# Performance work log

Measured on AMD Instinct MI355X. Metric: run time of the kernel, lower is better.

Reference implementation:

```python
import jax, jax.numpy as jnp
import numpy as np


def setup_inputs() -> dict:
    key = jax.random.key(0)
    ks = jax.random.split(key, 6)
    B, N, F = 32, 1000, 256
    x = jax.random.normal(ks[0], (B, N, F), jnp.float32)
    num_nodes = jax.random.randint(ks[1], (B,), 500, N + 1, dtype=jnp.int32)
    num_sentences = jax.random.randint(ks[2], (B,), 10, 100, dtype=jnp.int32)
    valid = (jnp.arange(N)[None, :] < num_nodes[:, None]).astype(jnp.float32)
    # sparse-like weighted adjacency (avg degree ~20), zeroed on padded rows/cols
    w = jax.random.uniform(ks[3], (B, N, N), jnp.float32)
    m = (jax.random.uniform(ks[4], (B, N, N)) < 0.02).astype(jnp.float32)
    adj = w * m * valid[:, :, None] * valid[:, None, :]
    W = jax.random.normal(ks[5], (F, 1), jnp.float32) * 0.1
    b = jnp.zeros((1,), jnp.float32)
    return dict(x=x, adj=adj, W=W, b=b, num_nodes=num_nodes,
                num_sentences=num_sentences, num_output_sentences=3)


def reference(x, adj, W, b, num_nodes, num_sentences, num_output_sentences):
    B, N, F = x.shape
    I = jnp.eye(N, dtype=x.dtype)
    valid = jnp.arange(N)[None, :] < num_nodes[:, None]  # [B,N]

    # --- GCNConv attention: sym-normalized (A_bin + I), out dim 1 ---
    A_bin = (adj > 0).astype(x.dtype)
    A_hat = A_bin + I
    dis = A_hat.sum(-1) ** -0.5  # deg >= 1 from self loops
    norm = dis[:, :, None] * A_hat * dis[:, None, :]
    alpha = jnp.einsum('bnm,bmf,fo->bno', norm, x, W)[..., 0] + b[0]
    alpha = jax.nn.sigmoid(alpha ** 2)           # pow(.,2) then sigmoid
    alpha = jnp.where(valid, alpha, -1.0)        # padded nodes sort last, cut to 0

    # --- top-k cutoff: keep highest-alpha nodes until num_output_sentences
    # sentence nodes (node index < num_sentences) have been seen ---
    order = jnp.argsort(-alpha, axis=-1)                      # descending
    is_sent = (order < num_sentences[:, None]).astype(jnp.int32)
    cum = jnp.cumsum(is_sent, axis=-1)
    cut_pos = jnp.argmax(cum >= num_output_sentences, axis=-1)  # first hit
    cut_node = jnp.take_along_axis(order, cut_pos[:, None], axis=1)
    cut_value = jnp.take_along_axis(alpha, cut_node, axis=1)     # [B,1]
    cut_alpha = jax.nn.relu(alpha + 1e-7 - cut_value)
    rank_mask = (jnp.arange(N)[None, :] <= cut_pos[:, None]).astype(x.dtype)
    index_mask = jnp.zeros_like(alpha).at[jnp.arange(B)[:, None], order].set(rank_mask)

    # --- normalize_batch_adj on the weighted adjacency ---
    A2 = adj + I
    d2 = jnp.clip(A2.sum(-1), 1.0) ** -0.5
    normA = d2[:, :, None] * A2 * d2[:, None, :]
    normA = (adj.sum(-1) > 0).astype(x.dtype)[:, :, None] * normA

    # --- assignment matrix S = row-L1-normalized (normA * cut_alpha[cols]) ---
    S = normA * cut_alpha[:, None, :]
    S = S / jnp.clip(jnp.sum(jnp.abs(S), axis=-1, keepdims=True), 1e-12)

    # --- coarsen: x' = S^T x ; A' = floor(S^T A S * 1e4)/1e4 ---
    x_c = jnp.einsum('bni,bnf->bif', S, x)
    coarse_adj = jnp.einsum('bim,bmj->bij', jnp.einsum('bni,bnm->bim', S, adj), S)
    coarse_adj = jnp.floor(coarse_adj * 1e4) / 1e4
    return x_c, coarse_adj, S, index_mask
```

## Files before the change

### kernel.cpp

```cpp
#include <hip/hip_runtime.h>
#include <math.h>
#include <limits.h>

#define CAP 64
#define TPB 256
#define RPB 4
#define NMAX 1024

typedef float f4 __attribute__((ext_vector_type(4)));

__device__ inline f4 ntload4(const float* p) { return __builtin_nontemporal_load((const f4*)p); }
__device__ inline void ntstore4(float* p, f4 v) { __builtin_nontemporal_store(v, (f4*)p); }
__device__ inline void ntstore1(float* p, float v) { __builtin_nontemporal_store(v, p); }

__device__ inline float waveSum(float v) {
#pragma unroll
  for (int o = 32; o > 0; o >>= 1) v += __shfl_down(v, o, 64);
  return v;
}

__global__ void k_prep(const float* __restrict__ x, const float* __restrict__ adj,
                       const float* __restrict__ W, float* __restrict__ y,
                       int* __restrict__ rowCnt, int* __restrict__ rowIdx,
                       float* __restrict__ rowVal, float* __restrict__ dis,
                       float* __restrict__ d2, float* __restrict__ wsum,
                       int* __restrict__ colCount, int* __restrict__ colK,
                       int N, int F, int BN, int B) {
  int wave = threadIdx.x >> 6, lane = threadIdx.x & 63;
  if (blockIdx.x == 0 && threadIdx.x < B) colK[threadIdx.x] = 0;
  int bn = blockIdx.x * RPB + wave;
  if (bn >= BN) return;
  if (lane == 0) colCount[bn] = 0;
  float p = 0.f;
  if ((F & 3) == 0) {
    const float* xr = x + (size_t)bn * F;
    int f4n = F >> 2;
    for (int i = lane; i < f4n; i += 64) {
      f4 a = *(const f4*)(xr + 4 * i);
      f4 w = *(const f4*)(W + 4 * i);
      p += a.x * w.x + a.y * w.y + a.z * w.z + a.w * w.w;
    }
  } else {
    for (int f = lane; f < F; f += 64) p += x[(size_t)bn * F + f] * W[f];
  }
  float ydot = waveSum(p);
  const float* row = adj + (size_t)bn * N;
  size_t lbase = (size_t)bn * CAP;
  unsigned long long below = (1ULL << lane) - 1ULL;
  float ls = 0.f;
  int cnt = 0;
  if ((N & 3) == 0) {
    int n4 = N >> 2;
    for (int q = lane; q < n4; q += 64) {
      f4 v = ntload4(row + 4 * q);
      ls += v.x + v.y + v.z + v.w;
      int j = q << 2;
#pragma unroll
      for (int c = 0; c < 4; c++) {
        float vc = (c == 0) ? v.x : (c == 1) ? v.y : (c == 2) ? v.z : v.w;
        unsigned long long m = __ballot(vc > 0.f);
        if (vc > 0.f) {
          int pos = cnt + __popcll(m & below);
          if (pos < CAP) { rowIdx[lbase + pos] = j + c; rowVal[lbase + pos] = vc; }
        }
        cnt += __popcll(m);
      }
    }
  } else {
    for (int j = lane; j < N; j += 64) {
      float v = row[j];
      ls += v;
      unsigned long long m = __ballot(v > 0.f);
      if (v > 0.f) {
        int pos = cnt + __popcll(m & below);
        if (pos < CAP) { rowIdx[lbase + pos] = j; rowVal[lbase + pos] = v; }
      }
      cnt += __popcll(m);
    }
  }
  float s = waveSum(ls);
  if (lane == 0) {
    y[bn] = ydot;
    rowCnt[bn] = cnt;
    dis[bn] = 1.f / sqrtf((float)(cnt + 1));
    wsum[bn] = s;
    d2[bn] = 1.f / sqrtf(fmaxf(s + 1.f, 1.f));
  }
}

__global__ void k_alpha(const float* __restrict__ adj, const int* __restrict__ rowCnt,
                        const int* __restrict__ rowIdx, const float* __restrict__ dis,
                        const float* __restrict__ y, const float* __restrict__ bptr,
                        const int* __restrict__ num_nodes, float* __restrict__ alpha,
                        int N, int BN) {
  int wave = threadIdx.x >> 6, lane = threadIdx.x & 63;
  int bn = blockIdx.x * RPB + wave;
  if (bn >= BN) return;
  int b = bn / N, n = bn - b * N;
  const float* disB = dis + (size_t)b * N;
  const float* yB = y + (size_t)b * N;
  int cnt = rowCnt[bn];
  float acc = 0.f;
  if (cnt <= CAP) {
    for (int t = lane; t < cnt; t += 64) {
      int j = rowIdx[(size_t)bn * CAP + t];
      acc += disB[j] * yB[j];
    }
  } else {
    const float* row = adj + (size_t)bn * N;
    for (int j = lane; j < N; j += 64)
      if (row[j] > 0.f) acc += disB[j] * yB[j];
  }
  float tot = waveSum(acc);
  if (lane == 0) {
    float dn = dis[bn];
    tot += dn * yB[n];
    float z = dn * tot + bptr[0];
    float a;
    if (n < num_nodes[b]) { float z2 = z * z; a = 1.f / (1.f + expf(-z2)); }
    else a = -1.f;
    alpha[bn] = a;
  }
}

__global__ void k_cut(const float* __restrict__ alpha, const int* __restrict__ num_sentences,
                      const int* __restrict__ kptr, float* __restrict__ cutA,
                      float* __restrict__ outIM, int* __restrict__ colK,
                      int* __restrict__ colIdx, int N) {
  int b = blockIdx.x;
  const float* aB = alpha + (size_t)b * N;
  __shared__ float s_cutv;
  __shared__ int s_cutn;
  if (threadIdx.x < 64) {
    int lane = threadIdx.x;
    int ns = num_sentences[b];
    int k = kptr[0];
    if (k < 1) k = 1;
    if (k > ns) k = ns;
    unsigned long long used = 0ULL;
    float cv = 0.f; int cn = 0;
    int nslots = (ns + 63) >> 6;
    for (int r = 0; r < k; r++) {
      float bv = -3.4e38f; int bi = INT_MAX;
      for (int s = 0; s < nslots; s++) {
        int idx = lane + (s << 6);
        if (idx < ns && !((used >> s) & 1ULL)) {
          float v = aB[idx];
          if (v > bv || (v == bv && idx < bi)) { bv = v; bi = idx; }
        }
      }
#pragma unroll
      for (int o = 32; o > 0; o >>= 1) {
        float ov = __shfl_down(bv, o, 64);
        int oi = __shfl_down(bi, o, 64);
        if (ov > bv || (ov == bv && oi < bi)) { bv = ov; bi = oi; }
      }
      bv = __shfl(bv, 0, 64);
      bi = __shfl(bi, 0, 64);
      if ((bi & 63) == lane) used |= 1ULL << (bi >> 6);
      cv = bv; cn = bi;
    }
    if (lane == 0) { s_cutv = cv; s_cutn = cn; }
  }
  __syncthreads();
  float cutv = s_cutv;
  int cutn = s_cutn;
  for (int n = threadIdx.x; n < N; n += TPB) {
    float a = aB[n];
    float ca = fmaxf((a + 1e-7f) - cutv, 0.f);
    cutA[(size_t)b * N + n] = ca;
    ntstore1(&outIM[(size_t)b * N + n], (a > cutv || (a == cutv && n <= cutn)) ? 1.f : 0.f);
    if (ca > 0.f) {
      int p = atomicAdd(&colK[b], 1);
      colIdx[(size_t)b * N + p] = n;
    }
  }
}

__global__ void k_srow(const float* __restrict__ adj, const int* __restrict__ rowCnt,
                       const int* __restrict__ rowIdx, const float* __restrict__ rowVal,
                       const float* __restrict__ wsum, const float* __restrict__ d2,
                       const float* __restrict__ cutA, float* __restrict__ outS,
                       int* __restrict__ colCount, int* __restrict__ colR,
                       float* __restrict__ colV, int N, int BN) {
  int wave = threadIdx.x >> 6, lane = threadIdx.x & 63;
  int bn = blockIdx.x * RPB + wave;
  bool rowOK = bn < BN;
  __shared__ float srow[RPB][NMAX];
  float* my = srow[wave];
  if (rowOK) for (int j = lane; j < N; j += 64) my[j] = 0.f;
  if (rowOK && wsum[bn] > 0.f) {
    int b = bn / N, n = bn - b * N;
    int cnt = rowCnt[bn];
    const float* d2B = d2 + (size_t)b * N;
    const float* caB = cutA + (size_t)b * N;
    float d2n = d2[bn];
    if (cnt < CAP) {
      int t = lane;
      int j = -1; float a2 = 0.f;
      if (t < cnt) {
        j = rowIdx[(size_t)bn * CAP + t];
        float v = rowVal[(size_t)bn * CAP + t];
        a2 = v + (j == n ? 1.f : 0.f);
      }
      unsigned long long hasDiag = __ballot(t < cnt && j == n);
      if (t == cnt && hasDiag == 0ULL) { j = n; a2 = 1.f; }
      float sun = 0.f;
      if (j >= 0) {
        float ca = caB[j];
        if (ca > 0.f) sun = d2n * a2 * d2B[j] * ca;
        else j = -1;
      }
      float denom = __shfl(waveSum(sun), 0, 64);
      denom = fmaxf(denom, 1e-12f);
      if (j >= 0) {
        float s = sun / denom;
        my[j] = s;
        int cp = atomicAdd(&colCount[(size_t)b * N + j], 1);
        if (cp < CAP) {
          colR[((size_t)b * N + j) * CAP + cp] = n;
          colV[((size_t)b * N + j) * CAP + cp] = s;
        }
      }
    } else {
      const float* row = adj + (size_t)bn * N;
      float ls = 0.f;
      for (int j2 = lane; j2 < N; j2 += 64) {
        float v = row[j2];
        bool nz = (v > 0.f) || (j2 == n);
        float a2 = v + (j2 == n ? 1.f : 0.f);
        float ca = caB[j2];
        if (nz && ca > 0.f) ls += d2n * a2 * d2B[j2] * ca;
      }
      float denom = __shfl(waveSum(ls), 0, 64);
      denom = fmaxf(denom, 1e-12f);
      for (int j2 = lane; j2 < N; j2 += 64) {
        float v = row[j2];
        bool nz = (v > 0.f) || (j2 == n);
        float a2 = v + (j2 == n ? 1.f : 0.f);
        float ca = caB[j2];
        if (nz && ca > 0.f) {
          float s = (d2n * a2 * d2B[j2] * ca) / denom;
          my[j2] = s;
          int cp = atomicAdd(&colCount[(size_t)b * N + j2], 1);
          if (cp < CAP) {
            colR[((size_t)b * N + j2) * CAP + cp] = n;
            colV[((size_t)b * N + j2) * CAP + cp] = s;
          }
        }
      }
    }
  }
  if (rowOK) {
    float* dst = outS + (size_t)bn * N;
    if ((N & 3) == 0) {
      int nq = N >> 2;
      for (int q = lane; q < nq; q += 64) {
        f4 v = { my[4 * q], my[4 * q + 1], my[4 * q + 2], my[4 * q + 3] };
        ntstore4(dst + 4 * q, v);
      }
    } else {
      for (int j = lane; j < N; j += 64) ntstore1(&dst[j], my[j]);
    }
  }
}

__global__ void k_coarse(const float* __restrict__ adj, const float* __restrict__ x,
                         const float* __restrict__ cutA,
                         const int* __restrict__ rowCnt, const int* __restrict__ rowIdx,
                         const float* __restrict__ rowVal,
                         const int* __restrict__ colK, const int* __restrict__ colIdx,
                         const int* __restrict__ colCount, const int* __restrict__ colR,
                         const float* __restrict__ colV,
                         float* __restrict__ outXc, float* __restrict__ outC,
                         int N, int F) {
  int bn = blockIdx.x;
  int b = bn / N;
  float* xcRow = outXc + (size_t)bn * F;
  float* cRow = outC + (size_t)bn * N;
  bool v4N = (N & 3) == 0, v4F = (F & 3) == 0;
  int nq = N >> 2, fq = F >> 2;
  if (cutA[bn] <= 0.f) {
    f4 z4 = { 0.f, 0.f, 0.f, 0.f };
    if (v4F) for (int q = threadIdx.x; q < fq; q += TPB) ntstore4(xcRow + 4 * q, z4);
    else for (int f = threadIdx.x; f < F; f += TPB) ntstore1(&xcRow[f], 0.f);
    if (v4N) for (int q = threadIdx.x; q < nq; q += TPB) ntstore4(cRow + 4 * q, z4);
    else for (int j = threadIdx.x; j < N; j += TPB) ntstore1(&cRow[j], 0.f);
    return;
  }
  __shared__ float T[NMAX];
  __shared__ float crow[NMAX];
  __shared__ int eR[CAP];
  __shared__ float eV[CAP];
  __shared__ int eCnt[CAP];
  int cci = colCount[bn];
  if (cci > CAP) cci = CAP;
  for (int r = threadIdx.x; r < cci; r += TPB) {
    int n_r = colR[(size_t)bn * CAP + r];
    eR[r] = n_r;
    eV[r] = colV[(size_t)bn * CAP + r];
    eCnt[r] = rowCnt[(size_t)b * N + n_r];
  }
  for (int m = threadIdx.x; m < N; m += TPB) { T[m] = 0.f; crow[m] = 0.f; }
  __syncthreads();
  const float* xB = x + (size_t)b * N * F;
  for (int f = threadIdx.x; f < F; f += TPB) {
    float acc = 0.f;
    for (int r = 0; r < cci; r++) acc += eV[r] * xB[(size_t)eR[r] * F + f];
    ntstore1(&xcRow[f], acc);
  }
  for (int idx = threadIdx.x; idx < cci * CAP; idx += TPB) {
    int r = idx >> 6;
    int t = idx & (CAP - 1);
    int c = eCnt[r];
    if (c <= CAP && t < c) {
      size_t base = ((size_t)b * N + eR[r]) * CAP;
      atomicAdd(&T[rowIdx[base + t]], eV[r] * rowVal[base + t]);
    }
  }
  for (int r = 0; r < cci; r++) {
    if (eCnt[r] > CAP) {
      const float* arow = adj + ((size_t)b * N + eR[r]) * N;
      float v = eV[r];
      for (int m = threadIdx.x; m < N; m += TPB) {
        float a = arow[m];
        if (a != 0.f) atomicAdd(&T[m], v * a);
      }
    }
  }
  __syncthreads();
  int K = colK[b];
  for (int jj = threadIdx.x; jj < K; jj += TPB) {
    int j = colIdx[(size_t)b * N + jj];
    int cj = colCount[(size_t)b * N + j];
    if (cj > CAP) cj = CAP;
    const int* jR = colR + ((size_t)b * N + j) * CAP;
    const float* jV = colV + ((size_t)b * N + j) * CAP;
    float cc = 0.f;
    for (int p = 0; p < cj; p++) cc += T[jR[p]] * jV[p];
    crow[j] = floorf(cc * 1e4f) / 1e4f;
  }
  __syncthreads();
  if (v4N) {
    for (int q = threadIdx.x; q < nq; q += TPB) {
      f4 v = { crow[4 * q], crow[4 * q + 1], crow[4 * q + 2], crow[4 * q + 3] };
      ntstore4(cRow + 4 * q, v);
    }
  } else {
    for (int j = threadIdx.x; j < N; j += TPB) ntstore1(&cRow[j], crow[j]);
  }
}

extern "C" void kernel_launch(void* const* d_in, const int* in_sizes, int n_in,
                              void* d_out, int out_size, void* d_ws, size_t ws_size,
                              hipStream_t stream) {
  const float* x = (const float*)d_in[0];
  const float* adj = (const float*)d_in[1];
  const float* W = (const float*)d_in[2];
  const float* bias = (const float*)d_in[3];
  const int* num_nodes = (const int*)d_in[4];
  const int* num_sentences = (const int*)d_in[5];
  const int* kptr = (const int*)d_in[6];

  int F = in_sizes[2];
  int B = in_sizes[4];
  int N = (int)(in_sizes[0] / ((long long)B * F));
  size_t BN = (size_t)B * N;

  float* outXc = (float*)d_out;
  float* outC = outXc + BN * F;
  float* outS = outC + BN * N;
  float* outIM = outS + BN * N;

  char* p = (char*)d_ws;
  auto alloc = [&](size_t bytes) -> void* {
    void* r = (void*)p;
    p += (bytes + 255) / 256 * 256;
    return r;
  };
  float* y = (float*)alloc(BN * 4);
  float* dis = (float*)alloc(BN * 4);
  float* d2 = (float*)alloc(BN * 4);
  float* wsum = (float*)alloc(BN * 4);
  float* alpha = (float*)alloc(BN * 4);
  float* cutA = (float*)alloc(BN * 4);
  int* rowCnt = (int*)alloc(BN * 4);
  int* rowIdx = (int*)alloc(BN * CAP * 4);
  float* rowVal = (float*)alloc(BN * CAP * 4);
  int* colCount = (int*)alloc(BN * 4);
  int* colR = (int*)alloc(BN * CAP * 4);
  float* colV = (float*)alloc(BN * CAP * 4);
  int* colK = (int*)alloc(B * 4);
  int* colIdx = (int*)alloc(BN * 4);

  int BNi = (int)BN;
  int rowBlocks = (BNi + RPB - 1) / RPB;
  k_prep<<<dim3(rowBlocks), dim3(TPB), 0, stream>>>(x, adj, W, y, rowCnt, rowIdx, rowVal,
                                                    dis, d2, wsum, colCount, colK, N, F, BNi, B);
  k_alpha<<<dim3(rowBlocks), dim3(TPB), 0, stream>>>(adj, rowCnt, rowIdx, dis, y, bias,
                                                     num_nodes, alpha, N, BNi);
  k_cut<<<dim3(B), dim3(TPB), 0, stream>>>(alpha, num_sentences, kptr, cutA, outIM, colK, colIdx, N);
  k_srow<<<dim3(rowBlocks), dim3(TPB), 0, stream>>>(adj, rowCnt, rowIdx, rowVal, wsum, d2, cutA,
                                                    outS, colCount, colR, colV, N, BNi);
  k_coarse<<<dim3(BNi), dim3(TPB), 0, stream>>>(adj, x, cutA, rowCnt, rowIdx, rowVal,
                                                colK, colIdx, colCount, colR, colV,
                                                outXc, outC, N, F);
}
```

Baseline: 443.3 us.

## Fuse alpha and cut kernels via last-block-per-batch atomic completion counter

Merges the alpha computation and the per-batch top-k cutoff into one kernel. Each block atomically adds its finished row count to a per-batch counter, and whichever block completes a batch runs that batch's cutoff selection and mask writes. This removes one kernel launch and the extra pass over alpha, but adds atomics and threadfences, and it leaves most blocks idle while a few serially process whole batches. It also vectorizes the shared-memory zeroing and the readback of rows in k_srow and k_coarse with float4 accesses.

```diff
diff --git a/kernel.cpp b/kernel.cpp
--- a/kernel.cpp
+++ b/kernel.cpp
@@ -25,9 +25,10 @@
                        float* __restrict__ rowVal, float* __restrict__ dis,
                        float* __restrict__ d2, float* __restrict__ wsum,
                        int* __restrict__ colCount, int* __restrict__ colK,
+                       int* __restrict__ batchDone,
                        int N, int F, int BN, int B) {
   int wave = threadIdx.x >> 6, lane = threadIdx.x & 63;
-  if (blockIdx.x == 0 && threadIdx.x < B) colK[threadIdx.x] = 0;
+  if (blockIdx.x == 0 && threadIdx.x < B) { colK[threadIdx.x] = 0; batchDone[threadIdx.x] = 0; }
   int bn = blockIdx.x * RPB + wave;
   if (bn >= BN) return;
   if (lane == 0) colCount[bn] = 0;
@@ -88,92 +89,116 @@
   }
 }
 
-__global__ void k_alpha(const float* __restrict__ adj, const int* __restrict__ rowCnt,
-                        const int* __restrict__ rowIdx, const float* __restrict__ dis,
-                        const float* __restrict__ y, const float* __restrict__ bptr,
-                        const int* __restrict__ num_nodes, float* __restrict__ alpha,
-                        int N, int BN) {
+__global__ void k_alpha_cut(const float* __restrict__ adj, const int* __restrict__ rowCnt,
+                            const int* __restrict__ rowIdx, const float* __restrict__ dis,
+                            const float* __restrict__ y, const float* __restrict__ bptr,
+                            const int* __restrict__ num_nodes,
+                            const int* __restrict__ num_sentences,
+                            const int* __restrict__ kptr,
+                            float* __restrict__ alpha, float* __restrict__ cutA,
+                            float* __restrict__ outIM, int* __restrict__ colK,
+                            int* __restrict__ colIdx, int* __restrict__ batchDone,
+                            int N, int BN) {
   int wave = threadIdx.x >> 6, lane = threadIdx.x & 63;
   int bn = blockIdx.x * RPB + wave;
-  if (bn >= BN) return;
-  int b = bn / N, n = bn - b * N;
-  const float* disB = dis + (size_t)b * N;
-  const float* yB = y + (size_t)b * N;
-  int cnt = rowCnt[bn];
-  float acc = 0.f;
-  if (cnt <= CAP) {
-    for (int t = lane; t < cnt; t += 64) {
-      int j = rowIdx[(size_t)bn * CAP + t];
-      acc += disB[j] * yB[j];
-    }
-  } else {
-    const float* row = adj + (size_t)bn * N;
-    for (int j = lane; j < N; j += 64)
-      if (row[j] > 0.f) acc += disB[j] * yB[j];
-  }
-  float tot = waveSum(acc);
-  if (lane == 0) {
-    float dn = dis[bn];
-    tot += dn * yB[n];
-    float z = dn * tot + bptr[0];
-    float a;
-    if (n < num_nodes[b]) { float z2 = z * z; a = 1.f / (1.f + expf(-z2)); }
-    else a = -1.f;
-    alpha[bn] = a;
-  }
-}
-
-__global__ void k_cut(const float* __restrict__ alpha, const int* __restrict__ num_sentences,
-                      const int* __restrict__ kptr, float* __restrict__ cutA,
-                      float* __restrict__ outIM, int* __restrict__ colK,
-                      int* __restrict__ colIdx, int N) {
-  int b = blockIdx.x;
-  const float* aB = alpha + (size_t)b * N;
-  __shared__ float s_cutv;
-  __shared__ int s_cutn;
-  if (threadIdx.x < 64) {
-    int lane = threadIdx.x;
-    int ns = num_sentences[b];
-    int k = kptr[0];
-    if (k < 1) k = 1;
-    if (k > ns) k = ns;
-    unsigned long long used = 0ULL;
-    float cv = 0.f; int cn = 0;
-    int nslots = (ns + 63) >> 6;
-    for (int r = 0; r < k; r++) {
-      float bv = -3.4e38f; int bi = INT_MAX;
-      for (int s = 0; s < nslots; s++) {
-        int idx = lane + (s << 6);
-        if (idx < ns && !((used >> s) & 1ULL)) {
-          float v = aB[idx];
-          if (v > bv || (v == bv && idx < bi)) { bv = v; bi = idx; }
+  if (bn < BN) {
+    int b = bn / N, n = bn - b * N;
+    const float* disB = dis + (size_t)b * N;
+    const float* yB = y + (size_t)b * N;
+    int cnt = rowCnt[bn];
+    float acc = 0.f;
+    if (cnt <= CAP) {
+      for (int t = lane; t < cnt; t += 64) {
+        int j = rowIdx[(size_t)bn * CAP + t];
+        acc += disB[j] * yB[j];
+      }
+    } else {
+      const float* row = adj + (size_t)bn * N;
+      for (int j = lane; j < N; j += 64)
+        if (row[j] > 0.f) acc += disB[j] * yB[j];
+    }
+    float tot = waveSum(acc);
+    if (lane == 0) {
+      float dn = dis[bn];
+      tot += dn * yB[n];
+      float z = dn * tot + bptr[0];
+      float a;
+      if (n < num_nodes[b]) { float z2 = z * z; a = 1.f / (1.f + expf(-z2)); }
+      else a = -1.f;
+      alpha[bn] = a;
+    }
+  }
+  __shared__ int winB[2];
+  __syncthreads();
+  if (threadIdx.x == 0) {
+    winB[0] = winB[1] = -1;
+    int start = blockIdx.x * RPB;
+    int end = start + RPB; if (end > BN) end = BN;
+    int i = start, w = 0;
+    __threadfence();
+    while (i < end) {
+      int b = i / N;
+      int segEnd = (b + 1) * N; if (segEnd > end) segEnd = end;
+      int c = segEnd - i;
+      int old = atomicAdd(&batchDone[b], c);
+      if (old + c == N && w < 2) winB[w++] = b;
+      i = segEnd;
+    }
+  }
+  __syncthreads();
+#pragma unroll
+  for (int w = 0; w < 2; w++) {
+    int b = winB[w];
+    if (b < 0) continue;
+    __threadfence();
+    const float* aB = alpha + (size_t)b * N;
+    __shared__ float s_cutv;
+    __shared__ int s_cutn;
+    if (threadIdx.x < 64) {
+      int ln = threadIdx.x;
+      int ns = num_sentences[b];
+      int k = kptr[0];
+      if (k < 1) k = 1;
+      if (k > ns) k = ns;
+      unsigned long long used = 0ULL;
+      float cv = 0.f; int cn = 0;
+      int nslots = (ns + 63) >> 6;
+      for (int r = 0; r < k; r++) {
+        float bv = -3.4e38f; int bi = INT_MAX;
+        for (int s = 0; s < nslots; s++) {
+          int idx = ln + (s << 6);
+          if (idx < ns && !((used >> s) & 1ULL)) {
+            float v = aB[idx];
+            if (v > bv || (v == bv && idx < bi)) { bv = v; bi = idx; }
+          }
         }
-      }
 #pragma unroll
-      for (int o = 32; o > 0; o >>= 1) {
-        float ov = __shfl_down(bv, o, 64);
-        int oi = __shfl_down(bi, o, 64);
-        if (ov > bv || (ov == bv && oi < bi)) { bv = ov; bi = oi; }
-      }
-      bv = __shfl(bv, 0, 64);
-      bi = __shfl(bi, 0, 64);
-      if ((bi & 63) == lane) used |= 1ULL << (bi >> 6);
-      cv = bv; cn = bi;
-    }
-    if (lane == 0) { s_cutv = cv; s_cutn = cn; }
-  }
-  __syncthreads();
-  float cutv = s_cutv;
-  int cutn = s_cutn;
-  for (int n = threadIdx.x; n < N; n += TPB) {
-    float a = aB[n];
-    float ca = fmaxf((a + 1e-7f) - cutv, 0.f);
-    cutA[(size_t)b * N + n] = ca;
-    ntstore1(&outIM[(size_t)b * N + n], (a > cutv || (a == cutv && n <= cutn)) ? 1.f : 0.f);
-    if (ca > 0.f) {
-      int p = atomicAdd(&colK[b], 1);
-      colIdx[(size_t)b * N + p] = n;
-    }
+        for (int o = 32; o > 0; o >>= 1) {
+          float ov = __shfl_down(bv, o, 64);
+          int oi = __shfl_down(bi, o, 64);
+          if (ov > bv || (ov == bv && oi < bi)) { bv = ov; bi = oi; }
+        }
+        bv = __shfl(bv, 0, 64);
+        bi = __shfl(bi, 0, 64);
+        if ((bi & 63) == ln) used |= 1ULL << (bi >> 6);
+        cv = bv; cn = bi;
+      }
+      if (ln == 0) { s_cutv = cv; s_cutn = cn; }
+    }
+    __syncthreads();
+    float cutv = s_cutv;
+    int cutn = s_cutn;
+    for (int n = threadIdx.x; n < N; n += TPB) {
+      float a = aB[n];
+      float ca = fmaxf((a + 1e-7f) - cutv, 0.f);
+      cutA[(size_t)b * N + n] = ca;
+      ntstore1(&outIM[(size_t)b * N + n], (a > cutv || (a == cutv && n <= cutn)) ? 1.f : 0.f);
+      if (ca > 0.f) {
+        int p = atomicAdd(&colK[b], 1);
+        colIdx[(size_t)b * N + p] = n;
+      }
+    }
+    __syncthreads();
   }
 }
 
@@ -188,7 +213,12 @@
   bool rowOK = bn < BN;
   __shared__ float srow[RPB][NMAX];
   float* my = srow[wave];
-  if (rowOK) for (int j = lane; j < N; j += 64) my[j] = 0.f;
+  if (rowOK) {
+    f4 z4 = { 0.f, 0.f, 0.f, 0.f };
+    int nq = N >> 2;
+    for (int q = lane; q < nq; q += 64) *(f4*)&my[4 * q] = z4;
+    for (int j = (nq << 2) + lane; j < N; j += 64) my[j] = 0.f;
+  }
   if (rowOK && wsum[bn] > 0.f) {
     int b = bn / N, n = bn - b * N;
     int cnt = rowCnt[bn];
@@ -255,10 +285,7 @@
     float* dst = outS + (size_t)bn * N;
     if ((N & 3) == 0) {
       int nq = N >> 2;
-      for (int q = lane; q < nq; q += 64) {
-        f4 v = { my[4 * q], my[4 * q + 1], my[4 * q + 2], my[4 * q + 3] };
-        ntstore4(dst + 4 * q, v);
-      }
+      for (int q = lane; q < nq; q += 64) ntstore4(dst + 4 * q, *(const f4*)&my[4 * q]);
     } else {
       for (int j = lane; j < N; j += 64) ntstore1(&dst[j], my[j]);
     }
@@ -342,10 +369,7 @@
   }
   __syncthreads();
   if (v4N) {
-    for (int q = threadIdx.x; q < nq; q += TPB) {
-      f4 v = { crow[4 * q], crow[4 * q + 1], crow[4 * q + 2], crow[4 * q + 3] };
-      ntstore4(cRow + 4 * q, v);
-    }
+    for (int q = threadIdx.x; q < nq; q += TPB) ntstore4(cRow + 4 * q, *(const f4*)&crow[4 * q]);
   } else {
     for (int j = threadIdx.x; j < N; j += TPB) ntstore1(&cRow[j], crow[j]);
   }
@@ -392,14 +416,17 @@
   float* colV = (float*)alloc(BN * CAP * 4);
   int* colK = (int*)alloc(B * 4);
   int* colIdx = (int*)alloc(BN * 4);
+  int* batchDone = (int*)alloc(B * 4);
 
   int BNi = (int)BN;
   int rowBlocks = (BNi + RPB - 1) / RPB;
   k_prep<<<dim3(rowBlocks), dim3(TPB), 0, stream>>>(x, adj, W, y, rowCnt, rowIdx, rowVal,
-                                                    dis, d2, wsum, colCount, colK, N, F, BNi, B);
-  k_alpha<<<dim3(rowBlocks), dim3(TPB), 0, stream>>>(adj, rowCnt, rowIdx, dis, y, bias,
-                                                     num_nodes, alpha, N, BNi);
-  k_cut<<<dim3(B), dim3(TPB), 0, stream>>>(alpha, num_sentences, kptr, cutA, outIM, colK, colIdx, N);
+                                                    dis, d2, wsum, colCount, colK, batchDone,
+                                                    N, F, BNi, B);
+  k_alpha_cut<<<dim3(rowBlocks), dim3(TPB), 0, stream>>>(adj, rowCnt, rowIdx, dis, y, bias,
+                                                         num_nodes, num_sentences, kptr,
+                                                         alpha, cutA, outIM, colK, colIdx,
+                                                         batchDone, N, BNi);
   k_srow<<<dim3(rowBlocks), dim3(TPB), 0, stream>>>(adj, rowCnt, rowIdx, rowVal, wsum, d2, cutA,
                                                     outS, colCount, colR, colV, N, BNi);
   k_coarse<<<dim3(BNi), dim3(TPB), 0, stream>>>(adj, x, cutA, rowCnt, rowIdx, rowVal,
```

Result: slower. 603.9 us (+36.2%).
